# Optimization experiments

Hardware: AMD Instinct MI355X
Metric: run time of the kernel (lower is better)

Reference implementation:

```python
import jax, jax.numpy as jnp
import numpy as np
from jax import lax

B, T, L = 16, 256, 1024       # batch, seq_length, input_size
NF = 32                        # num_filters
KS = [3, 5, 7]                 # kernel_sizes
H = 1024                       # feature_size
GRU_IN = NF * len(KS)          # 96


def setup_inputs() -> dict:
    key = jax.random.key(0)
    ks = jax.random.split(key, 20)
    def rn(k, shape, scale):
        return (jax.random.normal(k, shape, dtype=jnp.float32) * scale)
    inp = {
        "x": jax.random.normal(ks[0], (B, T, L), dtype=jnp.float32),
        "conv_w3": rn(ks[1], (NF, 1, 3), (2.0 / 3) ** 0.5),
        "conv_b3": jnp.zeros((NF,), jnp.float32),
        "conv_w5": rn(ks[2], (NF, 1, 5), (2.0 / 5) ** 0.5),
        "conv_b5": jnp.zeros((NF,), jnp.float32),
        "conv_w7": rn(ks[3], (NF, 1, 7), (2.0 / 7) ** 0.5),
        "conv_b7": jnp.zeros((NF,), jnp.float32),
        "gru_w_ih": rn(ks[4], (3 * H, GRU_IN), GRU_IN ** -0.5),
        "gru_w_hh": rn(ks[5], (3 * H, H), H ** -0.5),
        "gru_b_ih": jnp.zeros((3 * H,), jnp.float32),
        "gru_b_hh": jnp.zeros((3 * H,), jnp.float32),
        "attn_w1": rn(ks[6], (H, H), H ** -0.5),
        "attn_b1": jnp.zeros((H,), jnp.float32),
        "attn_w2": rn(ks[7], (1, H), H ** -0.5),
        "attn_b2": jnp.zeros((1,), jnp.float32),
        "fi_w1": rn(ks[8], (H, H), H ** -0.5),
        "fi_b1": jnp.zeros((H,), jnp.float32),
        "fi_w2": rn(ks[9], (H, H), H ** -0.5),
        "fi_b2": jnp.zeros((H,), jnp.float32),
        "lateral": jnp.full((H, H), 0.1, jnp.float32),
    }
    return inp


def _forward(x, conv_w3, conv_b3, conv_w5, conv_b5, conv_w7, conv_b7,
             gru_w_ih, gru_w_hh, gru_b_ih, gru_b_hh,
             attn_w1, attn_b1, attn_w2, attn_b2,
             fi_w1, fi_b1, fi_w2, fi_b2, lateral):
    b, t, l = x.shape
    # --- per-timestep conv branches (no cross-time dependence -> vectorize over B*T) ---
    xt = x.reshape(b * t, 1, l)  # (BT, C=1, L)
    pooled = []
    for w, bias in ((conv_w3, conv_b3), (conv_w5, conv_b5), (conv_w7, conv_b7)):
        y = lax.conv_general_dilated(xt, w, (1,), "SAME",
                                     dimension_numbers=("NCH", "OIH", "NCH"))
        y = jax.nn.relu(y + bias[None, :, None])
        pooled.append(jnp.max(y, axis=-1))  # adaptive_max_pool1d -> (BT, NF)
    feat = jnp.concatenate(pooled, axis=1).reshape(b, t, -1)  # (B, T, 3*NF)

    # --- GRU over time (sequential carry) ---
    gates_x = jnp.einsum("bti,gi->btg", feat, gru_w_ih) + gru_b_ih  # (B,T,3H)

    def step(h, gx):
        gh = h @ gru_w_hh.T + gru_b_hh
        xr, xz, xn = jnp.split(gx, 3, axis=-1)
        hr, hz, hn = jnp.split(gh, 3, axis=-1)
        r = jax.nn.sigmoid(xr + hr)
        z = jax.nn.sigmoid(xz + hz)
        n = jnp.tanh(xn + r * hn)
        h_new = (1.0 - z) * n + z * h
        return h_new, h_new

    h0 = jnp.zeros((b, gru_w_hh.shape[1]), x.dtype)
    _, hs = lax.scan(step, h0, jnp.swapaxes(gates_x, 0, 1))  # (T,B,H)
    hs = jnp.swapaxes(hs, 0, 1)  # (B,T,H)

    # --- attention: per-step softmax over a length-1 axis -> weights are all 1 ---
    scores = jnp.tanh(hs @ attn_w1.T + attn_b1) @ attn_w2.T + attn_b2  # (B,T,1)
    attn = jax.nn.softmax(scores, axis=-1)  # softmax over singleton seq dim -> ones
    attended = hs * attn  # (B,T,H)

    # --- lateral inhibition + feature integration MLP ---
    inhib = attended - jax.nn.relu(jnp.einsum("bth,hf->btf", attended, lateral))
    features = jax.nn.relu(inhib @ fi_w1.T + fi_b1) @ fi_w2.T + fi_b2  # (B,T,H)
    return features, attn[..., 0]  # attention_weights (B,T)


def reference(x, conv_w3, conv_b3, conv_w5, conv_b5, conv_w7, conv_b7,
              gru_w_ih, gru_w_hh, gru_b_ih, gru_b_hh,
              attn_w1, attn_b1, attn_w2, attn_b2,
              fi_w1, fi_b1, fi_w2, fi_b2, lateral):
    return _forward(x, conv_w3, conv_b3, conv_w5, conv_b5, conv_w7, conv_b7,
                    gru_w_ih, gru_w_hh, gru_b_ih, gru_b_hh,
                    attn_w1, attn_b1, attn_w2, attn_b2,
                    fi_w1, fi_b1, fi_w2, fi_b2, lateral)
```

## Files before the change

kernel.cpp:

```cpp
#include <hip/hip_runtime.h>
#include <stdint.h>
#include <stddef.h>

#define B_   16
#define T_   256
#define L_   1024
#define H_   1024
#define G3_  3072
#define KIN_ 96

#define SENT_     0x7FC1
#define SENT_X2_  0x7FC17FC1u

typedef __attribute__((ext_vector_type(8))) __bf16 bf16x8;
typedef __attribute__((ext_vector_type(4))) float  f32x4;
typedef __attribute__((ext_vector_type(4))) int    i32x4;

static __device__ __forceinline__ unsigned short f2bf(float x) {
  unsigned int u = __builtin_bit_cast(unsigned int, x);
  u += 0x7FFFu + ((u >> 16) & 1u);
  return (unsigned short)(u >> 16);
}
static __device__ __forceinline__ float bf2f(unsigned short s) {
  unsigned int u = ((unsigned int)s) << 16;
  return __builtin_bit_cast(float, u);
}
static __device__ __forceinline__ unsigned sentmask(unsigned d) {
  const unsigned x = d ^ SENT_X2_;
  return (x - 0x00010001u) & ~x & 0x80008000u;
}

__global__ void prep_kernel(
    const float* __restrict__ whh,  unsigned short* __restrict__ whh_bf,
    const float* __restrict__ wih,  unsigned short* __restrict__ wih_bf,
    const float* __restrict__ fiw1, unsigned short* __restrict__ fiw1_bf,
    const float* __restrict__ fiw2, unsigned short* __restrict__ fiw2_bf,
    const float* __restrict__ lat,  unsigned short* __restrict__ latT_bf,
    unsigned short* __restrict__ hsbuf, float* __restrict__ attn_out) {
  const int N0 = G3_ * H_;
  const int N1 = N0 + G3_ * KIN_;
  const int N2 = N1 + H_ * H_;
  const int N3 = N2 + H_ * H_;
  const int N4 = N3 + H_ * H_;
  const int N5 = N4 + T_ * B_ * H_ / 2;
  const int N6 = N5 + B_ * H_ / 2;
  const int N7 = N6 + B_ * T_;
  int i = blockIdx.x * 256 + threadIdx.x;
  const int stride = gridDim.x * 256;
  unsigned int* hs32 = (unsigned int*)hsbuf;
  for (; i < N7; i += stride) {
    if (i < N0)      whh_bf[i] = f2bf(whh[i]);
    else if (i < N1) { const int j = i - N0; wih_bf[j]  = f2bf(wih[j]); }
    else if (i < N2) { const int j = i - N1; fiw1_bf[j] = f2bf(fiw1[j]); }
    else if (i < N3) { const int j = i - N2; fiw2_bf[j] = f2bf(fiw2[j]); }
    else if (i < N4) { const int j = i - N3; const int r = j >> 10, c = j & 1023;
                       latT_bf[(size_t)c * H_ + r] = f2bf(lat[j]); }
    else if (i < N5) { hs32[B_ * H_ / 2 + (i - N4)] = SENT_X2_; }
    else if (i < N6) { hs32[i - N5] = 0u; }
    else             { attn_out[i - N6] = 1.0f; }
  }
}

__global__ __launch_bounds__(256) void conv_kernel(
    const float* __restrict__ x,
    const float* __restrict__ w3, const float* __restrict__ b3,
    const float* __restrict__ w5, const float* __restrict__ b5,
    const float* __restrict__ w7, const float* __restrict__ b7,
    unsigned short* __restrict__ feat) {
  __shared__ float xpad[L_ + 8];
  __shared__ float wlds[96][8];
  __shared__ float blds[96];
  __shared__ float wmax[4][96];
  const int tid = threadIdx.x;
  const int rid = blockIdx.x;
  const int b = rid >> 8;
  const int t = rid & 255;
  const float* xr = x + (size_t)rid * L_;
  for (int off = tid; off < L_; off += 256) xpad[off + 3] = xr[off];
  if (tid < 3) xpad[tid] = 0.f;
  if (tid >= 3 && tid < 8) xpad[L_ + tid] = 0.f;
  if (tid < 96) {
    const int f = tid;
    float wv[8];
#pragma unroll
    for (int k = 0; k < 8; ++k) wv[k] = 0.f;
    float bv;
    if (f < 32)      { for (int k = 0; k < 3; ++k) wv[k + 2] = w3[f * 3 + k]; bv = b3[f]; }
    else if (f < 64) { int ff = f - 32; for (int k = 0; k < 5; ++k) wv[k + 1] = w5[ff * 5 + k]; bv = b5[ff]; }
    else             { int ff = f - 64; for (int k = 0; k < 7; ++k) wv[k] = w7[ff * 7 + k]; bv = b7[ff]; }
#pragma unroll
    for (int k = 0; k < 8; ++k) wlds[f][k] = wv[k];
    blds[f] = bv;
  }
  __syncthreads();
  const int w = tid >> 6, lane = tid & 63;
  const int p0 = w * 256 + lane * 4;
  float xv[10];
#pragma unroll
  for (int i = 0; i < 10; ++i) xv[i] = xpad[p0 + i];
  for (int f = 0; f < 96; ++f) {
    float a0 = 0.f, a1 = 0.f, a2 = 0.f, a3 = 0.f;
#pragma unroll
    for (int k = 0; k < 7; ++k) {
      const float wk = wlds[f][k];
      a0 = fmaf(wk, xv[k],     a0);
      a1 = fmaf(wk, xv[k + 1], a1);
      a2 = fmaf(wk, xv[k + 2], a2);
      a3 = fmaf(wk, xv[k + 3], a3);
    }
    float m = fmaxf(fmaxf(a0, a1), fmaxf(a2, a3));
#pragma unroll
    for (int d = 1; d < 64; d <<= 1) m = fmaxf(m, __shfl_xor(m, d, 64));
    if (lane == 0) wmax[w][f] = m;
  }
  __syncthreads();
  if (tid < 96) {
    float m = fmaxf(fmaxf(wmax[0][tid], wmax[1][tid]),
                    fmaxf(wmax[2][tid], wmax[3][tid]));
    m += blds[tid];
    m = m > 0.f ? m : 0.f;
    feat[(size_t)(t * B_ + b) * KIN_ + tid] = f2bf(m);
  }
}

template <int EP>
__global__ __launch_bounds__(256) void gemm_kernel(
    const unsigned short* __restrict__ A,
    const unsigned short* __restrict__ Bm,
    int M, int N, int K, int lda, int ldb,
    const float* __restrict__ bias,
    float* __restrict__ outF,
    unsigned short* __restrict__ outB) {
  __shared__ __align__(16) unsigned short As[2][128 * 40];
  __shared__ __align__(16) unsigned short Bs[2][128 * 40];
  const int tid = threadIdx.x;
  const int n0 = blockIdx.x * 128;
  const int m0 = blockIdx.y * 128;
  const int w = tid >> 6;
  const int l = tid & 63;
  const int lr = l & 15;
  const int lk = (l >> 4) * 8;
  const int srow = tid >> 2;
  const int skc = (tid & 3) * 8;

  f32x4 acc[2][8];
#pragma unroll
  for (int i = 0; i < 2; ++i)
#pragma unroll
    for (int j = 0; j < 8; ++j) acc[i][j] = (f32x4){0.f, 0.f, 0.f, 0.f};

  const int NK = K >> 5;
  const unsigned short* Aptr  = A  + (size_t)(m0 + srow)      * lda + skc;
  const unsigned short* Aptr2 = A  + (size_t)(m0 + 64 + srow) * lda + skc;
  const unsigned short* Bptr  = Bm + (size_t)(n0 + srow)      * ldb + skc;
  const unsigned short* Bptr2 = Bm + (size_t)(n0 + 64 + srow) * ldb + skc;

  i32x4 ar0 = *(const i32x4*)(Aptr);
  i32x4 ar1 = *(const i32x4*)(Aptr2);
  i32x4 br0 = *(const i32x4*)(Bptr);
  i32x4 br1 = *(const i32x4*)(Bptr2);
  *(i32x4*)&As[0][srow * 40 + skc]        = ar0;
  *(i32x4*)&As[0][(64 + srow) * 40 + skc] = ar1;
  *(i32x4*)&Bs[0][srow * 40 + skc]        = br0;
  *(i32x4*)&Bs[0][(64 + srow) * 40 + skc] = br1;
  __syncthreads();

  for (int kk = 0; kk < NK; ++kk) {
    const int cur = kk & 1;
    if (kk + 1 < NK) {
      const int ko = (kk + 1) << 5;
      ar0 = *(const i32x4*)(Aptr  + ko);
      ar1 = *(const i32x4*)(Aptr2 + ko);
      br0 = *(const i32x4*)(Bptr  + ko);
      br1 = *(const i32x4*)(Bptr2 + ko);
    }
    const bf16x8 a0 = *(const bf16x8*)&As[cur][(w * 32 + lr) * 40 + lk];
    const bf16x8 a1 = *(const bf16x8*)&As[cur][(w * 32 + 16 + lr) * 40 + lk];
#pragma unroll
    for (int nt = 0; nt < 8; ++nt) {
      const bf16x8 bb = *(const bf16x8*)&Bs[cur][(nt * 16 + lr) * 40 + lk];
      acc[0][nt] = __builtin_amdgcn_mfma_f32_16x16x32_bf16(a0, bb, acc[0][nt], 0, 0, 0);
      acc[1][nt] = __builtin_amdgcn_mfma_f32_16x16x32_bf16(a1, bb, acc[1][nt], 0, 0, 0);
    }
    __syncthreads();
    if (kk + 1 < NK) {
      const int nxt = cur ^ 1;
      *(i32x4*)&As[nxt][srow * 40 + skc]        = ar0;
      *(i32x4*)&As[nxt][(64 + srow) * 40 + skc] = ar1;
      *(i32x4*)&Bs[nxt][srow * 40 + skc]        = br0;
      *(i32x4*)&Bs[nxt][(64 + srow) * 40 + skc] = br1;
    }
    __syncthreads();
  }

#pragma unroll
  for (int mt = 0; mt < 2; ++mt) {
#pragma unroll
    for (int nt = 0; nt < 8; ++nt) {
      const f32x4 v = acc[mt][nt];
      const int gcol = n0 + nt * 16 + lr;
#pragma unroll
      for (int e = 0; e < 4; ++e) {
        const int grow = m0 + w * 32 + mt * 16 + (l >> 4) * 4 + e;
        const float val = v[e];
        if (EP == 0) {
          outF[(size_t)grow * N + gcol] = val + bias[gcol];
        } else if (EP == 1) {
          const float hsv = bf2f(A[(size_t)grow * lda + gcol]);
          outB[(size_t)grow * N + gcol] = f2bf(hsv - fmaxf(val, 0.f));
        } else if (EP == 2) {
          outB[(size_t)grow * N + gcol] = f2bf(fmaxf(val + bias[gcol], 0.f));
        } else {
          const int tt = grow >> 4;
          const int bb2 = grow & 15;
          outF[((size_t)bb2 * T_ + tt) * H_ + gcol] = val + bias[gcol];
        }
      }
    }
  }
}

__global__ __launch_bounds__(512, 2) void gru_scan_kernel(
    const unsigned short* __restrict__ Whh,
    const float* __restrict__ gates,
    const float* __restrict__ bhh,
    unsigned short* __restrict__ hs) {
  const int g = blockIdx.x;
  const int tid = threadIdx.x;

  __shared__ float ghp[2][8][3][16][17];
  const int w = tid >> 6;
  const int l = tid & 63;
  const int lr = l & 15;
  const int lk8 = (l >> 4) * 8;
  const int j0 = g * 16;

  const unsigned short* ap0 = Whh + (size_t)(j0 + lr) * H_ + w * 128 + lk8;
  const unsigned short* ap1 = ap0 + (size_t)H_ * H_;
  const unsigned short* ap2 = ap1 + (size_t)H_ * H_;
  i32x4 w00, w01, w02, w03, w10, w11, w12, w13, w20, w21, w22, w23;
  asm volatile(
      "global_load_dwordx4 %0,  %12, off\n\t"
      "global_load_dwordx4 %1,  %12, off offset:64\n\t"
      "global_load_dwordx4 %2,  %12, off offset:128\n\t"
      "global_load_dwordx4 %3,  %12, off offset:192\n\t"
      "global_load_dwordx4 %4,  %13, off\n\t"
      "global_load_dwordx4 %5,  %13, off offset:64\n\t"
      "global_load_dwordx4 %6,  %13, off offset:128\n\t"
      "global_load_dwordx4 %7,  %13, off offset:192\n\t"
      "global_load_dwordx4 %8,  %14, off\n\t"
      "global_load_dwordx4 %9,  %14, off offset:64\n\t"
      "global_load_dwordx4 %10, %14, off offset:128\n\t"
      "global_load_dwordx4 %11, %14, off offset:192\n\t"
      "s_waitcnt vmcnt(0)"
      : "=&v"(w00), "=&v"(w01), "=&v"(w02), "=&v"(w03),
        "=&v"(w10), "=&v"(w11), "=&v"(w12), "=&v"(w13),
        "=&v"(w20), "=&v"(w21), "=&v"(w22), "=&v"(w23)
      : "v"(ap0), "v"(ap1), "v"(ap2));
  const bf16x8 af00 = __builtin_bit_cast(bf16x8, w00);
  const bf16x8 af01 = __builtin_bit_cast(bf16x8, w01);
  const bf16x8 af02 = __builtin_bit_cast(bf16x8, w02);
  const bf16x8 af03 = __builtin_bit_cast(bf16x8, w03);
  const bf16x8 af10 = __builtin_bit_cast(bf16x8, w10);
  const bf16x8 af11 = __builtin_bit_cast(bf16x8, w11);
  const bf16x8 af12 = __builtin_bit_cast(bf16x8, w12);
  const bf16x8 af13 = __builtin_bit_cast(bf16x8, w13);
  const bf16x8 af20 = __builtin_bit_cast(bf16x8, w20);
  const bf16x8 af21 = __builtin_bit_cast(bf16x8, w21);
  const bf16x8 af22 = __builtin_bit_cast(bf16x8, w22);
  const bf16x8 af23 = __builtin_bit_cast(bf16x8, w23);

  const int jb = tid & 15;
  const int bb = tid >> 4;
  const float bhr = bhh[j0 + jb];
  const float bhz = bhh[H_ + j0 + jb];
  const float bhn = bhh[2 * H_ + j0 + jb];
  float hprev = 0.f;

  for (int t = 0; t < T_; ++t) {
    const int buf = t & 1;
    float gxr = 0.f, gxz = 0.f, gxn = 0.f;
    if (tid < 256) {
      const size_t grow = ((size_t)t * B_ + bb) * G3_;
      gxr = gates[grow + j0 + jb];
      gxz = gates[grow + H_ + j0 + jb];
      gxn = gates[grow + 2 * H_ + j0 + jb];
    }

    const unsigned short* hp = hs + (size_t)t * (B_ * H_) +
                               (size_t)lr * H_ + w * 128 + lk8;
    i32x4 u0, u1, u2, u3;
    while (true) {
      asm volatile(
          "global_load_dwordx4 %0, %4, off sc0 sc1\n\t"
          "global_load_dwordx4 %1, %4, off offset:64 sc0 sc1\n\t"
          "global_load_dwordx4 %2, %4, off offset:128 sc0 sc1\n\t"
          "global_load_dwordx4 %3, %4, off offset:192 sc0 sc1\n\t"
          "s_waitcnt vmcnt(0)"
          : "=&v"(u0), "=&v"(u1), "=&v"(u2), "=&v"(u3)
          : "v"(hp)
          : "memory");
      const unsigned bad = sentmask(u0[0]) | sentmask(u0[3]) |
                           sentmask(u1[0]) | sentmask(u1[3]) |
                           sentmask(u2[0]) | sentmask(u2[3]) |
                           sentmask(u3[0]) | sentmask(u3[3]);
      if (__ballot(bad == 0) == ~0ull) break;
    }
    const bf16x8 hf0 = __builtin_bit_cast(bf16x8, u0);
    const bf16x8 hf1 = __builtin_bit_cast(bf16x8, u1);
    const bf16x8 hf2 = __builtin_bit_cast(bf16x8, u2);
    const bf16x8 hf3 = __builtin_bit_cast(bf16x8, u3);

    f32x4 C0 = (f32x4){0.f, 0.f, 0.f, 0.f}, C1 = C0, C2 = C0;
    C0 = __builtin_amdgcn_mfma_f32_16x16x32_bf16(af00, hf0, C0, 0, 0, 0);
    C1 = __builtin_amdgcn_mfma_f32_16x16x32_bf16(af10, hf0, C1, 0, 0, 0);
    C2 = __builtin_amdgcn_mfma_f32_16x16x32_bf16(af20, hf0, C2, 0, 0, 0);
    C0 = __builtin_amdgcn_mfma_f32_16x16x32_bf16(af01, hf1, C0, 0, 0, 0);
    C1 = __builtin_amdgcn_mfma_f32_16x16x32_bf16(af11, hf1, C1, 0, 0, 0);
    C2 = __builtin_amdgcn_mfma_f32_16x16x32_bf16(af21, hf1, C2, 0, 0, 0);
    C0 = __builtin_amdgcn_mfma_f32_16x16x32_bf16(af02, hf2, C0, 0, 0, 0);
    C1 = __builtin_amdgcn_mfma_f32_16x16x32_bf16(af12, hf2, C1, 0, 0, 0);
    C2 = __builtin_amdgcn_mfma_f32_16x16x32_bf16(af22, hf2, C2, 0, 0, 0);
    C0 = __builtin_amdgcn_mfma_f32_16x16x32_bf16(af03, hf3, C0, 0, 0, 0);
    C1 = __builtin_amdgcn_mfma_f32_16x16x32_bf16(af13, hf3, C1, 0, 0, 0);
    C2 = __builtin_amdgcn_mfma_f32_16x16x32_bf16(af23, hf3, C2, 0, 0, 0);

    const int rb = (l >> 4) * 4;
#pragma unroll
    for (int e = 0; e < 4; ++e) {
      ghp[buf][w][0][lr][rb + e] = C0[e];
      ghp[buf][w][1][lr][rb + e] = C1[e];
      ghp[buf][w][2][lr][rb + e] = C2[e];
    }
    __syncthreads();

    if (tid < 256) {
      float sr = bhr, sz = bhz, sn = bhn;
#pragma unroll
      for (int w2 = 0; w2 < 8; ++w2) {
        sr += ghp[buf][w2][0][bb][jb];
        sz += ghp[buf][w2][1][bb][jb];
        sn += ghp[buf][w2][2][bb][jb];
      }
      const float r = 1.f / (1.f + __expf(-(gxr + sr)));
      const float z = 1.f / (1.f + __expf(-(gxz + sz)));
      const float xn = gxn + r * sn;
      const float n = 2.f / (1.f + __expf(-2.f * xn)) - 1.f;
      const float hnew = (1.f - z) * n + z * hprev;
      hprev = hnew;

      const unsigned hv = (unsigned)f2bf(hnew);
      const int base = l & ~7;
      const unsigned s0 = __shfl(hv, base + 0, 64);
      const unsigned s1 = __shfl(hv, base + 1, 64);
      const unsigned s2 = __shfl(hv, base + 2, 64);
      const unsigned s3 = __shfl(hv, base + 3, 64);
      const unsigned s4 = __shfl(hv, base + 4, 64);
      const unsigned s5 = __shfl(hv, base + 5, 64);
      const unsigned s6 = __shfl(hv, base + 6, 64);
      const unsigned s7 = __shfl(hv, base + 7, 64);
      i32x4 pk;
      pk[0] = (int)(s0 | (s1 << 16));
      pk[1] = (int)(s2 | (s3 << 16));
      pk[2] = (int)(s4 | (s5 << 16));
      pk[3] = (int)(s6 | (s7 << 16));
      if ((l & 7) == 0) {
        unsigned short* sp = hs + ((size_t)(t + 1) * B_ + bb) * H_ + j0 + (l & 15);
        asm volatile("global_store_dwordx4 %0, %1, off sc0 sc1"
                     :: "v"(sp), "v"(pk) : "memory");
      }
    }
  }
}

extern "C" void kernel_launch(void* const* d_in, const int* in_sizes, int n_in,
                              void* d_out, int out_size, void* d_ws, size_t ws_size,
                              hipStream_t stream) {
  (void)in_sizes; (void)n_in; (void)out_size; (void)ws_size;
  const float* x    = (const float*)d_in[0];
  const float* w3   = (const float*)d_in[1];
  const float* b3   = (const float*)d_in[2];
  const float* w5   = (const float*)d_in[3];
  const float* b5   = (const float*)d_in[4];
  const float* w7   = (const float*)d_in[5];
  const float* b7   = (const float*)d_in[6];
  const float* wih  = (const float*)d_in[7];
  const float* whh  = (const float*)d_in[8];
  const float* bih  = (const float*)d_in[9];
  const float* bhh  = (const float*)d_in[10];
  const float* fiw1 = (const float*)d_in[15];
  const float* fib1 = (const float*)d_in[16];
  const float* fiw2 = (const float*)d_in[17];
  const float* fib2 = (const float*)d_in[18];
  const float* lat  = (const float*)d_in[19];

  char* ws = (char*)d_ws;
  size_t off = 0;
  auto alloc = [&](size_t bytes) -> void* {
    void* p = ws + off;
    off += (bytes + 255) & ~(size_t)255;
    return p;
  };
  unsigned short* whh_bf  = (unsigned short*)alloc((size_t)G3_ * H_ * 2);
  unsigned short* wih_bf  = (unsigned short*)alloc((size_t)G3_ * KIN_ * 2);
  unsigned short* latT_bf = (unsigned short*)alloc((size_t)H_ * H_ * 2);
  unsigned short* fiw1_bf = (unsigned short*)alloc((size_t)H_ * H_ * 2);
  unsigned short* fiw2_bf = (unsigned short*)alloc((size_t)H_ * H_ * 2);
  unsigned short* feat_bf = (unsigned short*)alloc((size_t)B_ * T_ * KIN_ * 2);
  float*          gates   = (float*)alloc((size_t)B_ * T_ * G3_ * 4);
  unsigned short* hsbuf   = (unsigned short*)alloc((size_t)(T_ + 1) * B_ * H_ * 2);
  unsigned short* inhib   = (unsigned short*)alloc((size_t)B_ * T_ * H_ * 2);
  unsigned short* y1      = (unsigned short*)alloc((size_t)B_ * T_ * H_ * 2);

  prep_kernel<<<4096, 256, 0, stream>>>(whh, whh_bf, wih, wih_bf,
                                        fiw1, fiw1_bf, fiw2, fiw2_bf,
                                        lat, latT_bf, hsbuf,
                                        (float*)d_out + (size_t)B_ * T_ * H_);

  conv_kernel<<<B_ * T_, 256, 0, stream>>>(x, w3, b3, w5, b5, w7, b7, feat_bf);

  {
    dim3 grid(G3_ / 128, (B_ * T_) / 128);
    gemm_kernel<0><<<grid, 256, 0, stream>>>(feat_bf, wih_bf, B_ * T_, G3_, KIN_,
                                             KIN_, KIN_, bih, gates, nullptr);
  }

  gru_scan_kernel<<<64, 512, 0, stream>>>(whh_bf, gates, bhh, hsbuf);

  const unsigned short* hs1 = hsbuf + (size_t)B_ * H_;
  {
    dim3 grid(H_ / 128, (B_ * T_) / 128);
    gemm_kernel<1><<<grid, 256, 0, stream>>>(hs1, latT_bf, B_ * T_, H_, H_,
                                             H_, H_, nullptr, nullptr, inhib);
    gemm_kernel<2><<<grid, 256, 0, stream>>>(inhib, fiw1_bf, B_ * T_, H_, H_,
                                             H_, H_, fib1, nullptr, y1);
    gemm_kernel<3><<<grid, 256, 0, stream>>>(y1, fiw2_bf, B_ * T_, H_, H_,
                                             H_, H_, fib2, (float*)d_out, nullptr);
  }
}
```

Before: 1.064 ms.

## Fuse input-gate GEMM into GRU scan and merge prep with conv kernel

Computes the input-to-hidden gate projection inside the GRU scan kernel with MFMA on the fly, one step ahead, so the separate input GEMM and its fp32 gates buffer round-trip are gone. Merges the weight-conversion prep kernel and the conv kernel into one launch that splits work by block index. Issues the next step's hidden-state loads speculatively before the step ends so the polling latency overlaps with work. This adds MFMA work and LDS traffic to the serial recurrent loop. If the speculative load reads sentinels, the kernel falls back to polling.

```diff
diff --git a/kernel.cpp b/kernel.cpp
--- a/kernel.cpp
+++ b/kernel.cpp
@@ -8,6 +8,7 @@
 #define H_   1024
 #define G3_  3072
 #define KIN_ 96
+#define CONVB_ 4096
 
 #define SENT_     0x7FC1
 #define SENT_X2_  0x7FC17FC1u
@@ -30,48 +31,50 @@
   return (x - 0x00010001u) & ~x & 0x80008000u;
 }
 
-__global__ void prep_kernel(
+__global__ __launch_bounds__(256) void prep_conv_kernel(
+    const float* __restrict__ x,
+    const float* __restrict__ w3, const float* __restrict__ b3,
+    const float* __restrict__ w5, const float* __restrict__ b5,
+    const float* __restrict__ w7, const float* __restrict__ b7,
+    unsigned short* __restrict__ feat,
     const float* __restrict__ whh,  unsigned short* __restrict__ whh_bf,
     const float* __restrict__ wih,  unsigned short* __restrict__ wih_bf,
     const float* __restrict__ fiw1, unsigned short* __restrict__ fiw1_bf,
     const float* __restrict__ fiw2, unsigned short* __restrict__ fiw2_bf,
     const float* __restrict__ lat,  unsigned short* __restrict__ latT_bf,
     unsigned short* __restrict__ hsbuf, float* __restrict__ attn_out) {
-  const int N0 = G3_ * H_;
-  const int N1 = N0 + G3_ * KIN_;
-  const int N2 = N1 + H_ * H_;
-  const int N3 = N2 + H_ * H_;
-  const int N4 = N3 + H_ * H_;
-  const int N5 = N4 + T_ * B_ * H_ / 2;
-  const int N6 = N5 + B_ * H_ / 2;
-  const int N7 = N6 + B_ * T_;
-  int i = blockIdx.x * 256 + threadIdx.x;
-  const int stride = gridDim.x * 256;
-  unsigned int* hs32 = (unsigned int*)hsbuf;
-  for (; i < N7; i += stride) {
-    if (i < N0)      whh_bf[i] = f2bf(whh[i]);
-    else if (i < N1) { const int j = i - N0; wih_bf[j]  = f2bf(wih[j]); }
-    else if (i < N2) { const int j = i - N1; fiw1_bf[j] = f2bf(fiw1[j]); }
-    else if (i < N3) { const int j = i - N2; fiw2_bf[j] = f2bf(fiw2[j]); }
-    else if (i < N4) { const int j = i - N3; const int r = j >> 10, c = j & 1023;
-                       latT_bf[(size_t)c * H_ + r] = f2bf(lat[j]); }
-    else if (i < N5) { hs32[B_ * H_ / 2 + (i - N4)] = SENT_X2_; }
-    else if (i < N6) { hs32[i - N5] = 0u; }
-    else             { attn_out[i - N6] = 1.0f; }
-  }
-}
-
-__global__ __launch_bounds__(256) void conv_kernel(
-    const float* __restrict__ x,
-    const float* __restrict__ w3, const float* __restrict__ b3,
-    const float* __restrict__ w5, const float* __restrict__ b5,
-    const float* __restrict__ w7, const float* __restrict__ b7,
-    unsigned short* __restrict__ feat) {
   __shared__ float xpad[L_ + 8];
   __shared__ float wlds[96][8];
   __shared__ float blds[96];
   __shared__ float wmax[4][96];
   const int tid = threadIdx.x;
+
+  if (blockIdx.x >= CONVB_) {
+    const int N0 = G3_ * H_;
+    const int N1 = N0 + G3_ * KIN_;
+    const int N2 = N1 + H_ * H_;
+    const int N3 = N2 + H_ * H_;
+    const int N4 = N3 + H_ * H_;
+    const int N5 = N4 + T_ * B_ * H_ / 2;
+    const int N6 = N5 + B_ * H_ / 2;
+    const int N7 = N6 + B_ * T_;
+    int i = (blockIdx.x - CONVB_) * 256 + tid;
+    const int stride = (gridDim.x - CONVB_) * 256;
+    unsigned int* hs32 = (unsigned int*)hsbuf;
+    for (; i < N7; i += stride) {
+      if (i < N0)      whh_bf[i] = f2bf(whh[i]);
+      else if (i < N1) { const int j = i - N0; wih_bf[j]  = f2bf(wih[j]); }
+      else if (i < N2) { const int j = i - N1; fiw1_bf[j] = f2bf(fiw1[j]); }
+      else if (i < N3) { const int j = i - N2; fiw2_bf[j] = f2bf(fiw2[j]); }
+      else if (i < N4) { const int j = i - N3; const int r = j >> 10, c = j & 1023;
+                         latT_bf[(size_t)c * H_ + r] = f2bf(lat[j]); }
+      else if (i < N5) { hs32[B_ * H_ / 2 + (i - N4)] = SENT_X2_; }
+      else if (i < N6) { hs32[i - N5] = 0u; }
+      else             { attn_out[i - N6] = 1.0f; }
+    }
+    return;
+  }
+
   const int rid = blockIdx.x;
   const int b = rid >> 8;
   const int t = rid & 255;
@@ -203,9 +206,7 @@
       for (int e = 0; e < 4; ++e) {
         const int grow = m0 + w * 32 + mt * 16 + (l >> 4) * 4 + e;
         const float val = v[e];
-        if (EP == 0) {
-          outF[(size_t)grow * N + gcol] = val + bias[gcol];
-        } else if (EP == 1) {
+        if (EP == 1) {
           const float hsv = bf2f(A[(size_t)grow * lda + gcol]);
           outB[(size_t)grow * N + gcol] = f2bf(hsv - fmaxf(val, 0.f));
         } else if (EP == 2) {
@@ -222,41 +223,50 @@
 
 __global__ __launch_bounds__(512, 2) void gru_scan_kernel(
     const unsigned short* __restrict__ Whh,
-    const float* __restrict__ gates,
+    const unsigned short* __restrict__ Wih,
+    const unsigned short* __restrict__ feat,
     const float* __restrict__ bhh,
+    const float* __restrict__ bih,
     unsigned short* __restrict__ hs) {
   const int g = blockIdx.x;
   const int tid = threadIdx.x;
 
   __shared__ float ghp[2][8][3][16][17];
+  __shared__ float gxS[2][3][16][17];
   const int w = tid >> 6;
   const int l = tid & 63;
   const int lr = l & 15;
   const int lk8 = (l >> 4) * 8;
   const int j0 = g * 16;
+  const int wg = (w < 3) ? w : 0;
 
   const unsigned short* ap0 = Whh + (size_t)(j0 + lr) * H_ + w * 128 + lk8;
   const unsigned short* ap1 = ap0 + (size_t)H_ * H_;
   const unsigned short* ap2 = ap1 + (size_t)H_ * H_;
-  i32x4 w00, w01, w02, w03, w10, w11, w12, w13, w20, w21, w22, w23;
+  const unsigned short* agp = Wih + (size_t)(wg * H_ + j0 + lr) * KIN_ + lk8;
+  i32x4 w00, w01, w02, w03, w10, w11, w12, w13, w20, w21, w22, w23, q0, q1, q2;
   asm volatile(
-      "global_load_dwordx4 %0,  %12, off\n\t"
-      "global_load_dwordx4 %1,  %12, off offset:64\n\t"
-      "global_load_dwordx4 %2,  %12, off offset:128\n\t"
-      "global_load_dwordx4 %3,  %12, off offset:192\n\t"
-      "global_load_dwordx4 %4,  %13, off\n\t"
-      "global_load_dwordx4 %5,  %13, off offset:64\n\t"
-      "global_load_dwordx4 %6,  %13, off offset:128\n\t"
-      "global_load_dwordx4 %7,  %13, off offset:192\n\t"
-      "global_load_dwordx4 %8,  %14, off\n\t"
-      "global_load_dwordx4 %9,  %14, off offset:64\n\t"
-      "global_load_dwordx4 %10, %14, off offset:128\n\t"
-      "global_load_dwordx4 %11, %14, off offset:192\n\t"
+      "global_load_dwordx4 %0,  %15, off\n\t"
+      "global_load_dwordx4 %1,  %15, off offset:64\n\t"
+      "global_load_dwordx4 %2,  %15, off offset:128\n\t"
+      "global_load_dwordx4 %3,  %15, off offset:192\n\t"
+      "global_load_dwordx4 %4,  %16, off\n\t"
+      "global_load_dwordx4 %5,  %16, off offset:64\n\t"
+      "global_load_dwordx4 %6,  %16, off offset:128\n\t"
+      "global_load_dwordx4 %7,  %16, off offset:192\n\t"
+      "global_load_dwordx4 %8,  %17, off\n\t"
+      "global_load_dwordx4 %9,  %17, off offset:64\n\t"
+      "global_load_dwordx4 %10, %17, off offset:128\n\t"
+      "global_load_dwordx4 %11, %17, off offset:192\n\t"
+      "global_load_dwordx4 %12, %18, off\n\t"
+      "global_load_dwordx4 %13, %18, off offset:64\n\t"
+      "global_load_dwordx4 %14, %18, off offset:128\n\t"
       "s_waitcnt vmcnt(0)"
       : "=&v"(w00), "=&v"(w01), "=&v"(w02), "=&v"(w03),
         "=&v"(w10), "=&v"(w11), "=&v"(w12), "=&v"(w13),
-        "=&v"(w20), "=&v"(w21), "=&v"(w22), "=&v"(w23)
-      : "v"(ap0), "v"(ap1), "v"(ap2));
+        "=&v"(w20), "=&v"(w21), "=&v"(w22), "=&v"(w23),
+        "=&v"(q0), "=&v"(q1), "=&v"(q2)
+      : "v"(ap0), "v"(ap1), "v"(ap2), "v"(agp));
   const bf16x8 af00 = __builtin_bit_cast(bf16x8, w00);
   const bf16x8 af01 = __builtin_bit_cast(bf16x8, w01);
   const bf16x8 af02 = __builtin_bit_cast(bf16x8, w02);
@@ -269,42 +279,69 @@
   const bf16x8 af21 = __builtin_bit_cast(bf16x8, w21);
   const bf16x8 af22 = __builtin_bit_cast(bf16x8, w22);
   const bf16x8 af23 = __builtin_bit_cast(bf16x8, w23);
+  const bf16x8 ga0  = __builtin_bit_cast(bf16x8, q0);
+  const bf16x8 ga1  = __builtin_bit_cast(bf16x8, q1);
+  const bf16x8 ga2  = __builtin_bit_cast(bf16x8, q2);
 
   const int jb = tid & 15;
   const int bb = tid >> 4;
+  const float bxr = bih[j0 + jb];
+  const float bxz = bih[H_ + j0 + jb];
+  const float bxn = bih[2 * H_ + j0 + jb];
   const float bhr = bhh[j0 + jb];
   const float bhz = bhh[H_ + j0 + jb];
   const float bhn = bhh[2 * H_ + j0 + jb];
   float hprev = 0.f;
+  const int rb = (l >> 4) * 4;
+
+  if (w < 3) {
+    const unsigned short* fp = feat + (size_t)lr * KIN_ + lk8;
+    const bf16x8 fb0 = *(const bf16x8*)(fp);
+    const bf16x8 fb1 = *(const bf16x8*)(fp + 32);
+    const bf16x8 fb2 = *(const bf16x8*)(fp + 64);
+    f32x4 G = (f32x4){0.f, 0.f, 0.f, 0.f};
+    G = __builtin_amdgcn_mfma_f32_16x16x32_bf16(ga0, fb0, G, 0, 0, 0);
+    G = __builtin_amdgcn_mfma_f32_16x16x32_bf16(ga1, fb1, G, 0, 0, 0);
+    G = __builtin_amdgcn_mfma_f32_16x16x32_bf16(ga2, fb2, G, 0, 0, 0);
+#pragma unroll
+    for (int e = 0; e < 4; ++e) gxS[0][w][lr][rb + e] = G[e];
+  }
+  __syncthreads();
+
+  i32x4 u0, u1, u2, u3;
+  int sv = 0;
 
   for (int t = 0; t < T_; ++t) {
     const int buf = t & 1;
-    float gxr = 0.f, gxz = 0.f, gxn = 0.f;
-    if (tid < 256) {
-      const size_t grow = ((size_t)t * B_ + bb) * G3_;
-      gxr = gates[grow + j0 + jb];
-      gxz = gates[grow + H_ + j0 + jb];
-      gxn = gates[grow + 2 * H_ + j0 + jb];
-    }
-
     const unsigned short* hp = hs + (size_t)t * (B_ * H_) +
                                (size_t)lr * H_ + w * 128 + lk8;
-    i32x4 u0, u1, u2, u3;
-    while (true) {
-      asm volatile(
-          "global_load_dwordx4 %0, %4, off sc0 sc1\n\t"
-          "global_load_dwordx4 %1, %4, off offset:64 sc0 sc1\n\t"
-          "global_load_dwordx4 %2, %4, off offset:128 sc0 sc1\n\t"
-          "global_load_dwordx4 %3, %4, off offset:192 sc0 sc1\n\t"
-          "s_waitcnt vmcnt(0)"
-          : "=&v"(u0), "=&v"(u1), "=&v"(u2), "=&v"(u3)
-          : "v"(hp)
-          : "memory");
+    int got = 0;
+    if (sv) {
+      asm volatile("s_waitcnt vmcnt(0)" ::: "memory");
+      __builtin_amdgcn_sched_barrier(0);
       const unsigned bad = sentmask(u0[0]) | sentmask(u0[3]) |
                            sentmask(u1[0]) | sentmask(u1[3]) |
                            sentmask(u2[0]) | sentmask(u2[3]) |
                            sentmask(u3[0]) | sentmask(u3[3]);
-      if (__ballot(bad == 0) == ~0ull) break;
+      got = (__ballot(bad == 0) == ~0ull) ? 1 : 0;
+    }
+    if (!got) {
+      while (true) {
+        asm volatile(
+            "global_load_dwordx4 %0, %4, off sc0 sc1\n\t"
+            "global_load_dwordx4 %1, %4, off offset:64 sc0 sc1\n\t"
+            "global_load_dwordx4 %2, %4, off offset:128 sc0 sc1\n\t"
+            "global_load_dwordx4 %3, %4, off offset:192 sc0 sc1\n\t"
+            "s_waitcnt vmcnt(0)"
+            : "=&v"(u0), "=&v"(u1), "=&v"(u2), "=&v"(u3)
+            : "v"(hp)
+            : "memory");
+        const unsigned bad = sentmask(u0[0]) | sentmask(u0[3]) |
+                             sentmask(u1[0]) | sentmask(u1[3]) |
+                             sentmask(u2[0]) | sentmask(u2[3]) |
+                             sentmask(u3[0]) | sentmask(u3[3]);
+        if (__ballot(bad == 0) == ~0ull) break;
+      }
     }
     const bf16x8 hf0 = __builtin_bit_cast(bf16x8, u0);
     const bf16x8 hf1 = __builtin_bit_cast(bf16x8, u1);
@@ -325,7 +362,6 @@
     C1 = __builtin_amdgcn_mfma_f32_16x16x32_bf16(af13, hf3, C1, 0, 0, 0);
     C2 = __builtin_amdgcn_mfma_f32_16x16x32_bf16(af23, hf3, C2, 0, 0, 0);
 
-    const int rb = (l >> 4) * 4;
 #pragma unroll
     for (int e = 0; e < 4; ++e) {
       ghp[buf][w][0][lr][rb + e] = C0[e];
@@ -335,16 +371,19 @@
     __syncthreads();
 
     if (tid < 256) {
-      float sr = bhr, sz = bhz, sn = bhn;
+      const float gxr = gxS[buf][0][bb][jb] + bxr;
+      const float gxz = gxS[buf][1][bb][jb] + bxz;
+      const float gxn = gxS[buf][2][bb][jb] + bxn;
+      float hr = bhr, hz = bhz, hn = bhn;
 #pragma unroll
       for (int w2 = 0; w2 < 8; ++w2) {
-        sr += ghp[buf][w2][0][bb][jb];
-        sz += ghp[buf][w2][1][bb][jb];
-        sn += ghp[buf][w2][2][bb][jb];
+        hr += ghp[buf][w2][0][bb][jb];
+        hz += ghp[buf][w2][1][bb][jb];
+        hn += ghp[buf][w2][2][bb][jb];
       }
-      const float r = 1.f / (1.f + __expf(-(gxr + sr)));
-      const float z = 1.f / (1.f + __expf(-(gxz + sz)));
-      const float xn = gxn + r * sn;
+      const float r = 1.f / (1.f + __expf(-(gxr + hr)));
+      const float z = 1.f / (1.f + __expf(-(gxz + hz)));
+      const float xn = gxn + r * hn;
       const float n = 2.f / (1.f + __expf(-2.f * xn)) - 1.f;
       const float hnew = (1.f - z) * n + z * hprev;
       hprev = hnew;
@@ -370,6 +409,32 @@
                      :: "v"(sp), "v"(pk) : "memory");
       }
     }
+
+    if (t + 1 < T_) {
+      if (w < 3) {
+        const unsigned short* fp = feat + (size_t)((t + 1) * B_ + lr) * KIN_ + lk8;
+        const bf16x8 fb0 = *(const bf16x8*)(fp);
+        const bf16x8 fb1 = *(const bf16x8*)(fp + 32);
+        const bf16x8 fb2 = *(const bf16x8*)(fp + 64);
+        f32x4 G = (f32x4){0.f, 0.f, 0.f, 0.f};
+        G = __builtin_amdgcn_mfma_f32_16x16x32_bf16(ga0, fb0, G, 0, 0, 0);
+        G = __builtin_amdgcn_mfma_f32_16x16x32_bf16(ga1, fb1, G, 0, 0, 0);
+        G = __builtin_amdgcn_mfma_f32_16x16x32_bf16(ga2, fb2, G, 0, 0, 0);
+#pragma unroll
+        for (int e = 0; e < 4; ++e) gxS[buf ^ 1][w][lr][rb + e] = G[e];
+      }
+      const unsigned short* hp2 = hs + (size_t)(t + 1) * (B_ * H_) +
+                                  (size_t)lr * H_ + w * 128 + lk8;
+      asm volatile(
+          "global_load_dwordx4 %0, %4, off sc0 sc1\n\t"
+          "global_load_dwordx4 %1, %4, off offset:64 sc0 sc1\n\t"
+          "global_load_dwordx4 %2, %4, off offset:128 sc0 sc1\n\t"
+          "global_load_dwordx4 %3, %4, off offset:192 sc0 sc1"
+          : "=&v"(u0), "=&v"(u1), "=&v"(u2), "=&v"(u3)
+          : "v"(hp2)
+          : "memory");
+      sv = 1;
+    }
   }
 }
 
@@ -407,25 +472,16 @@
   unsigned short* fiw1_bf = (unsigned short*)alloc((size_t)H_ * H_ * 2);
   unsigned short* fiw2_bf = (unsigned short*)alloc((size_t)H_ * H_ * 2);
   unsigned short* feat_bf = (unsigned short*)alloc((size_t)B_ * T_ * KIN_ * 2);
-  float*          gates   = (float*)alloc((size_t)B_ * T_ * G3_ * 4);
   unsigned short* hsbuf   = (unsigned short*)alloc((size_t)(T_ + 1) * B_ * H_ * 2);
   unsigned short* inhib   = (unsigned short*)alloc((size_t)B_ * T_ * H_ * 2);
   unsigned short* y1      = (unsigned short*)alloc((size_t)B_ * T_ * H_ * 2);
 
-  prep_kernel<<<4096, 256, 0, stream>>>(whh, whh_bf, wih, wih_bf,
-                                        fiw1, fiw1_bf, fiw2, fiw2_bf,
-                                        lat, latT_bf, hsbuf,
-                                        (float*)d_out + (size_t)B_ * T_ * H_);
-
-  conv_kernel<<<B_ * T_, 256, 0, stream>>>(x, w3, b3, w5, b5, w7, b7, feat_bf);
-
-  {
-    dim3 grid(G3_ / 128, (B_ * T_) / 128);
-    gemm_kernel<0><<<grid, 256, 0, stream>>>(feat_bf, wih_bf, B_ * T_, G3_, KIN_,
-                                             KIN_, KIN_, bih, gates, nullptr);
-  }
-
-  gru_scan_kernel<<<64, 512, 0, stream>>>(whh_bf, gates, bhh, hsbuf);
+  prep_conv_kernel<<<CONVB_ + 2048, 256, 0, stream>>>(
+      x, w3, b3, w5, b5, w7, b7, feat_bf,
+      whh, whh_bf, wih, wih_bf, fiw1, fiw1_bf, fiw2, fiw2_bf,
+      lat, latT_bf, hsbuf, (float*)d_out + (size_t)B_ * T_ * H_);
+
+  gru_scan_kernel<<<64, 512, 0, stream>>>(whh_bf, wih_bf, feat_bf, bhh, bih, hsbuf);
 
   const unsigned short* hs1 = hsbuf + (size_t)B_ * H_;
   {
```

Measured after the change: 1.103 ms. 3.7% more time.
